# Performance work log

Measured on AMD Instinct MI355X. Metric: run time of the kernel, lower is better.

Reference implementation:

```python
import jax, jax.numpy as jnp
import numpy as np


def setup_inputs() -> dict:
    key = jax.random.key(0)
    k1, k2, k3 = jax.random.split(key, 3)
    B, E, L, D = 32, 256, 2048, 256
    doc_state = jax.random.normal(k1, (B, L, D), dtype=jnp.float32)
    entity_mapping = jax.random.uniform(k2, (B, E, L), dtype=jnp.float32)
    entity_lens = jax.random.uniform(k3, (B, E), dtype=jnp.float32)
    return {"doc_state": doc_state, "entity_mapping": entity_mapping, "entity_lens": entity_lens}


def reference(doc_state, entity_mapping, entity_lens):
    # Original: (entity_mapping[:, :, :, None] * doc_state[:, None, :, :]).sum(2) / entity_lens[:, :, None]
    # This is a batched contraction over L; express as einsum to avoid the
    # huge [B, E, L, D] intermediate.
    summed = jnp.einsum('bel,bld->bed', entity_mapping, doc_state)  # [B, E, D]
    return summed / entity_lens[:, :, None]
```

## Files before the change

### kernel.cpp

```cpp
#include <hip/hip_runtime.h>
#include <stdint.h>

#define B_ 32
#define E_ 256
#define L_ 2048
#define D_ 256

#define BE 128
#define BD 256
#define BK 32
#define KS 4
#define KCHUNK (L_ / KS)
#define NKT (KCHUNK / BK)
#define SUP 128

typedef __attribute__((ext_vector_type(2))) float  f32x2;
typedef __attribute__((ext_vector_type(4))) float  f32x4;
typedef __attribute__((ext_vector_type(4))) short  s16x4;
typedef __attribute__((ext_vector_type(8))) short  s16x8;

#define KEYB(row) (((row) >> 1) & 7)

__device__ __forceinline__ void cvt_hilo1(float x, short &h, short &l) {
    unsigned u = __builtin_bit_cast(unsigned, x);
    h = (short)(u >> 16);
    float hf = __builtin_bit_cast(float, u & 0xFFFF0000u);
    unsigned r = __builtin_bit_cast(unsigned, x - hf);
    l = (short)(r >> 16);
}

__global__ void zero_out_kernel(f32x4* __restrict__ out) {
    out[(size_t)blockIdx.x * 256 + threadIdx.x] = f32x4{0.f, 0.f, 0.f, 0.f};
}

#define LOAD_A(RA, SS)                                                         \
    {                                                                          \
        _Pragma("unroll")                                                      \
        for (int rr = 0; rr < 8; ++rr)                                         \
            RA[rr] = *(const f32x4*)(Ag + (size_t)(rr * 16 + a_sr) * L_ + (SS) * SUP + a_sc * 4); \
    }

#define WRITE_A(RA)                                                            \
    {                                                                          \
        _Pragma("unroll")                                                      \
        for (int rr = 0; rr < 8; ++rr) {                                       \
            s16x4 h, l;                                                        \
            _Pragma("unroll")                                                  \
            for (int i = 0; i < 4; ++i) { short hh, ll; cvt_hilo1(RA[rr][i], hh, ll); h[i] = hh; l[i] = ll; } \
            *(s16x4*)&A_hi[awoff + rr * 2048] = h;                             \
            *(s16x4*)&A_lo[awoff + rr * 2048] = l;                             \
        }                                                                      \
    }

#define LOADT_B(PB, K0)                                                        \
    {                                                                          \
        _Pragma("unroll")                                                      \
        for (int j = 0; j < 8; ++j)                                            \
            PB[j] = *(const f32x2*)(Sg + (size_t)((K0) + kb * 8 + j) * D_ + dp * 2); \
    }

#define STAGE_B(BbN, PB)                                                       \
    {                                                                          \
        _Pragma("unroll")                                                      \
        for (int dd = 0; dd < 2; ++dd) {                                       \
            s16x8 h, l;                                                        \
            _Pragma("unroll")                                                  \
            for (int j = 0; j < 8; ++j) { short hh, ll; cvt_hilo1(PB[j][dd], hh, ll); h[j] = hh; l[j] = ll; } \
            *(s16x8*)&(BbN)[bwo_h[dd]] = h;                                    \
            *(s16x8*)&(BbN)[bwo_l[dd]] = l;                                    \
        }                                                                      \
    }

#define LGKM_BARRIER()                                                         \
    {                                                                          \
        asm volatile("s_waitcnt lgkmcnt(0)" ::: "memory");                     \
        __builtin_amdgcn_s_barrier();                                          \
        asm volatile("" ::: "memory");                                         \
    }

#define ITER(K, S, BbC, BbN, PB)                                               \
    {                                                                          \
        s16x8 bh[4], bl[4], ah[4], al[4];                                      \
        _Pragma("unroll")                                                      \
        for (int ni = 0; ni < 4; ++ni) {                                       \
            bh[ni] = *(const s16x8*)&(BbC)[bro_h[ni]];                         \
            bl[ni] = *(const s16x8*)&(BbC)[bro_l[ni]];                         \
        }                                                                      \
        _Pragma("unroll")                                                      \
        for (int mi = 0; mi < 4; ++mi) {                                       \
            const int aoff = abase[mi] + ((((S) * 4 + kg) ^ akey[mi]) << 3);   \
            ah[mi] = *(const s16x8*)&A_hi[aoff];                               \
            al[mi] = *(const s16x8*)&A_lo[aoff];                               \
        }                                                                      \
        if ((K) + 1 < NKT) {                                                   \
            STAGE_B(BbN, PB)                                                   \
            if ((K) + 3 < NKT) LOADT_B(PB, ((K) + 3) * BK)                     \
        }                                                                      \
        __builtin_amdgcn_s_setprio(1);                                         \
        _Pragma("unroll")                                                      \
        for (int mi = 0; mi < 4; ++mi)                                         \
            _Pragma("unroll")                                                  \
            for (int ni = 0; ni < 4; ++ni) {                                   \
                acc[mi][ni] = __builtin_amdgcn_mfma_f32_16x16x32_bf16(ah[mi], bh[ni], acc[mi][ni], 0, 0, 0); \
                acc[mi][ni] = __builtin_amdgcn_mfma_f32_16x16x32_bf16(ah[mi], bl[ni], acc[mi][ni], 0, 0, 0); \
                acc[mi][ni] = __builtin_amdgcn_mfma_f32_16x16x32_bf16(al[mi], bh[ni], acc[mi][ni], 0, 0, 0); \
            }                                                                  \
        __builtin_amdgcn_s_setprio(0);                                         \
        if ((K) + 1 < NKT) LGKM_BARRIER()                                      \
    }

__global__ __launch_bounds__(512, 2)
void mean_pool_kernel(const float* __restrict__ doc,
                      const float* __restrict__ emap,
                      const float* __restrict__ lens,
                      float* __restrict__ out) {
    __shared__ __align__(16) short A_hi[BE * SUP];
    __shared__ __align__(16) short A_lo[BE * SUP];
    __shared__ __align__(16) short Bs[2][BD][64];
    __shared__ float lens_s[BE];

    const int t  = threadIdx.x;
    const int bi = blockIdx.x;
    const int r   = bi & 7;
    const int q   = bi >> 3;
    const int ks  = r & 3;
    const int b   = (q >> 1) * 2 + (r >> 2);
    const int e0  = (q & 1) * BE;

    const float* Ag = emap + ((size_t)b * E_ + e0) * L_ + ks * KCHUNK;
    const float* Sg = doc  + (size_t)b * L_ * D_ + (size_t)ks * KCHUNK * D_;

    if (t < BE) lens_s[t] = lens[b * E_ + e0 + t];

    const int a_sr = t >> 5;
    const int a_sc = t & 31;
    const int akey_w = a_sr & 7;
    const int awoff = a_sr * SUP + (((a_sc >> 1) ^ akey_w) << 3) + (a_sc & 1) * 4;

    const int dp = t & 127;
    const int kb = t >> 7;

    const int lane = t & 63;
    const int w    = t >> 6;
    const int eo   = (w & 1) * 64;
    const int dq   = (w >> 1) * 32 * 2;
    const int ml   = lane & 15;
    const int kg   = lane >> 4;

    int bwo_h[2], bwo_l[2];
    #pragma unroll
    for (int dd = 0; dd < 2; ++dd) {
        const int row = dp * 2 + dd, k = KEYB(row);
        bwo_h[dd] = row * 64 + (((kb    ) ^ k) << 3);
        bwo_l[dd] = row * 64 + (((kb | 4) ^ k) << 3);
    }
    int abase[4], akey[4], bro_h[4], bro_l[4];
    #pragma unroll
    for (int i = 0; i < 4; ++i) {
        const int ar = eo + i * 16 + ml;
        abase[i] = ar * SUP;
        akey[i]  = ar & 7;
        const int br = dq + i * 16 + ml, kB = KEYB(br);
        bro_h[i] = br * 64 + (((kg    ) ^ kB) << 3);
        bro_l[i] = br * 64 + (((kg | 4) ^ kB) << 3);
    }

    f32x4 acc[4][4] = {};
    f32x4 ra[8];
    f32x2 pbE[8], pbO[8];

    LOAD_A(ra, 0)
    LOADT_B(pbE, 0)
    LOADT_B(pbO, BK)
    STAGE_B((&Bs[0][0][0]), pbE)
    LOADT_B(pbE, 2 * BK)

    for (int ss = 0; ss < 4; ++ss) {
        WRITE_A(ra)
        if (ss < 3) LOAD_A(ra, ss + 1)
        LGKM_BARRIER()

        const int kt = ss * 4;
        ITER(kt + 0, 0, (&Bs[0][0][0]), (&Bs[1][0][0]), pbO)
        ITER(kt + 1, 1, (&Bs[1][0][0]), (&Bs[0][0][0]), pbE)
        ITER(kt + 2, 2, (&Bs[0][0][0]), (&Bs[1][0][0]), pbO)
        ITER(kt + 3, 3, (&Bs[1][0][0]), (&Bs[0][0][0]), pbE)
    }

    #pragma unroll
    for (int mi = 0; mi < 4; ++mi) {
        #pragma unroll
        for (int rr = 0; rr < 4; ++rr) {
            const int er = eo + mi * 16 + kg * 4 + rr;
            const float lv = lens_s[er];
            #pragma unroll
            for (int ni = 0; ni < 4; ++ni)
                atomicAdd(&out[((size_t)(b * E_ + e0 + er)) * D_ + dq + ni * 16 + ml],
                          acc[mi][ni][rr] / lv);
        }
    }
}

extern "C" void kernel_launch(void* const* d_in, const int* in_sizes, int n_in,
                              void* d_out, int out_size, void* d_ws, size_t ws_size,
                              hipStream_t stream) {
    const float* doc  = (const float*)d_in[0];
    const float* emap = (const float*)d_in[1];
    const float* lens = (const float*)d_in[2];
    float* out = (float*)d_out;

    zero_out_kernel<<<dim3(out_size / (4 * 256)), dim3(256), 0, stream>>>((f32x4*)out);

    dim3 grid(B_ * (E_ / BE) * (D_ / BD) * KS);
    dim3 block(512);
    hipLaunchKernelGGL(mean_pool_kernel, grid, block, 0, stream,
                       doc, emap, lens, out);
}
```

Before: 180.3 us.

## Drop block barriers: per-warp private A LDS buffers and direct-register B fragments

Replaces the block-shared A tile and double-buffered shared B staging with per-warp private LDS buffers for A and direct global-to-register loads of B in MFMA fragment layout. All workgroup barriers are removed, so waves progress independently, and lens is read from global in the epilogue. The cost is scalar, strided B loads that are duplicated across the waves sharing a D range, which raises memory and cache traffic.

```diff
diff --git a/kernel.cpp b/kernel.cpp
--- a/kernel.cpp
+++ b/kernel.cpp
@@ -12,14 +12,10 @@
 #define KS 4
 #define KCHUNK (L_ / KS)
 #define NKT (KCHUNK / BK)
-#define SUP 128
 
-typedef __attribute__((ext_vector_type(2))) float  f32x2;
 typedef __attribute__((ext_vector_type(4))) float  f32x4;
 typedef __attribute__((ext_vector_type(4))) short  s16x4;
 typedef __attribute__((ext_vector_type(8))) short  s16x8;
-
-#define KEYB(row) (((row) >> 1) & 7)
 
 __device__ __forceinline__ void cvt_hilo1(float x, short &h, short &l) {
     unsigned u = __builtin_bit_cast(unsigned, x);
@@ -33,80 +29,65 @@
     out[(size_t)blockIdx.x * 256 + threadIdx.x] = f32x4{0.f, 0.f, 0.f, 0.f};
 }
 
-#define LOAD_A(RA, SS)                                                         \
+#define LOADA(RA, K0)                                                          \
     {                                                                          \
         _Pragma("unroll")                                                      \
-        for (int rr = 0; rr < 8; ++rr)                                         \
-            RA[rr] = *(const f32x4*)(Ag + (size_t)(rr * 16 + a_sr) * L_ + (SS) * SUP + a_sc * 4); \
+        for (int i = 0; i < 8; ++i)                                            \
+            RA[i] = *(const f32x4*)(AgW + (size_t)(i * 8 + arow) * L_ + (K0) + akq * 4); \
     }
 
-#define WRITE_A(RA)                                                            \
+#define LOADB(PB, K0)                                                          \
     {                                                                          \
         _Pragma("unroll")                                                      \
-        for (int rr = 0; rr < 8; ++rr) {                                       \
+        for (int ni = 0; ni < 4; ++ni)                                         \
+            _Pragma("unroll")                                                  \
+            for (int j = 0; j < 8; ++j)                                        \
+                PB[ni][j] = Sg[(size_t)((K0) + kg * 8 + j) * D_ + dq + ni * 16 + ml]; \
+    }
+
+#define CVTWRITE_A(AW, RA)                                                     \
+    {                                                                          \
+        _Pragma("unroll")                                                      \
+        for (int i = 0; i < 8; ++i) {                                          \
             s16x4 h, l;                                                        \
             _Pragma("unroll")                                                  \
-            for (int i = 0; i < 4; ++i) { short hh, ll; cvt_hilo1(RA[rr][i], hh, ll); h[i] = hh; l[i] = ll; } \
-            *(s16x4*)&A_hi[awoff + rr * 2048] = h;                             \
-            *(s16x4*)&A_lo[awoff + rr * 2048] = l;                             \
+            for (int q = 0; q < 4; ++q) { short hh, ll; cvt_hilo1(RA[i][q], hh, ll); h[q] = hh; l[q] = ll; } \
+            *(s16x4*)&(AW)[i * 256 + awoff]        = h;                        \
+            *(s16x4*)&(AW)[i * 256 + awoff + 2048] = l;                        \
         }                                                                      \
     }
 
-#define LOADT_B(PB, K0)                                                        \
+#define CVT_B(BH, BL, PB)                                                      \
     {                                                                          \
         _Pragma("unroll")                                                      \
-        for (int j = 0; j < 8; ++j)                                            \
-            PB[j] = *(const f32x2*)(Sg + (size_t)((K0) + kb * 8 + j) * D_ + dp * 2); \
+        for (int ni = 0; ni < 4; ++ni)                                         \
+            _Pragma("unroll")                                                  \
+            for (int j = 0; j < 8; ++j) {                                      \
+                short hh, ll; cvt_hilo1(PB[ni][j], hh, ll);                    \
+                BH[ni][j] = hh; BL[ni][j] = ll;                                \
+            }                                                                  \
     }
 
-#define STAGE_B(BbN, PB)                                                       \
+#define STEP(K, AW)                                                            \
     {                                                                          \
-        _Pragma("unroll")                                                      \
-        for (int dd = 0; dd < 2; ++dd) {                                       \
-            s16x8 h, l;                                                        \
-            _Pragma("unroll")                                                  \
-            for (int j = 0; j < 8; ++j) { short hh, ll; cvt_hilo1(PB[j][dd], hh, ll); h[j] = hh; l[j] = ll; } \
-            *(s16x8*)&(BbN)[bwo_h[dd]] = h;                                    \
-            *(s16x8*)&(BbN)[bwo_l[dd]] = l;                                    \
-        }                                                                      \
-    }
-
-#define LGKM_BARRIER()                                                         \
-    {                                                                          \
-        asm volatile("s_waitcnt lgkmcnt(0)" ::: "memory");                     \
-        __builtin_amdgcn_s_barrier();                                          \
-        asm volatile("" ::: "memory");                                         \
-    }
-
-#define ITER(K, S, BbC, BbN, PB)                                               \
-    {                                                                          \
-        s16x8 bh[4], bl[4], ah[4], al[4];                                      \
-        _Pragma("unroll")                                                      \
-        for (int ni = 0; ni < 4; ++ni) {                                       \
-            bh[ni] = *(const s16x8*)&(BbC)[bro_h[ni]];                         \
-            bl[ni] = *(const s16x8*)&(BbC)[bro_l[ni]];                         \
-        }                                                                      \
+        CVTWRITE_A(AW, ra)                                                     \
+        if ((K) + 1 < NKT) LOADA(ra, ((K) + 1) * BK)                           \
+        s16x8 bh[4], bl[4];                                                    \
+        CVT_B(bh, bl, pbv)                                                     \
+        if ((K) + 1 < NKT) LOADB(pbv, ((K) + 1) * BK)                          \
+        __builtin_amdgcn_s_setprio(1);                                         \
         _Pragma("unroll")                                                      \
         for (int mi = 0; mi < 4; ++mi) {                                       \
-            const int aoff = abase[mi] + ((((S) * 4 + kg) ^ akey[mi]) << 3);   \
-            ah[mi] = *(const s16x8*)&A_hi[aoff];                               \
-            al[mi] = *(const s16x8*)&A_lo[aoff];                               \
-        }                                                                      \
-        if ((K) + 1 < NKT) {                                                   \
-            STAGE_B(BbN, PB)                                                   \
-            if ((K) + 3 < NKT) LOADT_B(PB, ((K) + 3) * BK)                     \
-        }                                                                      \
-        __builtin_amdgcn_s_setprio(1);                                         \
-        _Pragma("unroll")                                                      \
-        for (int mi = 0; mi < 4; ++mi)                                         \
+            const s16x8 ah = *(const s16x8*)&(AW)[aoff[mi]];                   \
+            const s16x8 al = *(const s16x8*)&(AW)[aoff[mi] + 2048];            \
             _Pragma("unroll")                                                  \
             for (int ni = 0; ni < 4; ++ni) {                                   \
-                acc[mi][ni] = __builtin_amdgcn_mfma_f32_16x16x32_bf16(ah[mi], bh[ni], acc[mi][ni], 0, 0, 0); \
-                acc[mi][ni] = __builtin_amdgcn_mfma_f32_16x16x32_bf16(ah[mi], bl[ni], acc[mi][ni], 0, 0, 0); \
-                acc[mi][ni] = __builtin_amdgcn_mfma_f32_16x16x32_bf16(al[mi], bh[ni], acc[mi][ni], 0, 0, 0); \
+                acc[mi][ni] = __builtin_amdgcn_mfma_f32_16x16x32_bf16(ah, bh[ni], acc[mi][ni], 0, 0, 0); \
+                acc[mi][ni] = __builtin_amdgcn_mfma_f32_16x16x32_bf16(ah, bl[ni], acc[mi][ni], 0, 0, 0); \
+                acc[mi][ni] = __builtin_amdgcn_mfma_f32_16x16x32_bf16(al, bh[ni], acc[mi][ni], 0, 0, 0); \
             }                                                                  \
+        }                                                                      \
         __builtin_amdgcn_s_setprio(0);                                         \
-        if ((K) + 1 < NKT) LGKM_BARRIER()                                      \
     }
 
 __global__ __launch_bounds__(512, 2)
@@ -114,10 +95,7 @@
                       const float* __restrict__ emap,
                       const float* __restrict__ lens,
                       float* __restrict__ out) {
-    __shared__ __align__(16) short A_hi[BE * SUP];
-    __shared__ __align__(16) short A_lo[BE * SUP];
-    __shared__ __align__(16) short Bs[2][BD][64];
-    __shared__ float lens_s[BE];
+    __shared__ __align__(16) short Apriv[8][2][4096];
 
     const int t  = threadIdx.x;
     const int bi = blockIdx.x;
@@ -130,69 +108,50 @@
     const float* Ag = emap + ((size_t)b * E_ + e0) * L_ + ks * KCHUNK;
     const float* Sg = doc  + (size_t)b * L_ * D_ + (size_t)ks * KCHUNK * D_;
 
-    if (t < BE) lens_s[t] = lens[b * E_ + e0 + t];
-
-    const int a_sr = t >> 5;
-    const int a_sc = t & 31;
-    const int akey_w = a_sr & 7;
-    const int awoff = a_sr * SUP + (((a_sc >> 1) ^ akey_w) << 3) + (a_sc & 1) * 4;
-
-    const int dp = t & 127;
-    const int kb = t >> 7;
-
     const int lane = t & 63;
     const int w    = t >> 6;
     const int eo   = (w & 1) * 64;
-    const int dq   = (w >> 1) * 32 * 2;
+    const int dq   = (w >> 1) * 64;
     const int ml   = lane & 15;
     const int kg   = lane >> 4;
 
-    int bwo_h[2], bwo_l[2];
+    const float* AgW = Ag + (size_t)eo * L_;
+
+    const int arow = lane >> 3;
+    const int akq  = lane & 7;
+    const int awoff = (arow * 8 + (akq ^ (arow & 6))) * 4;
+
+    int aoff[4];
     #pragma unroll
-    for (int dd = 0; dd < 2; ++dd) {
-        const int row = dp * 2 + dd, k = KEYB(row);
-        bwo_h[dd] = row * 64 + (((kb    ) ^ k) << 3);
-        bwo_l[dd] = row * 64 + (((kb | 4) ^ k) << 3);
+    for (int mi = 0; mi < 4; ++mi) {
+        const int row = mi * 16 + ml;
+        const int r7  = row & 7;
+        const int slot = r7 * 8 + ((2 * kg) ^ (r7 & 6));
+        aoff[mi] = (row >> 3) * 256 + slot * 4;
     }
-    int abase[4], akey[4], bro_h[4], bro_l[4];
-    #pragma unroll
-    for (int i = 0; i < 4; ++i) {
-        const int ar = eo + i * 16 + ml;
-        abase[i] = ar * SUP;
-        akey[i]  = ar & 7;
-        const int br = dq + i * 16 + ml, kB = KEYB(br);
-        bro_h[i] = br * 64 + (((kg    ) ^ kB) << 3);
-        bro_l[i] = br * 64 + (((kg | 4) ^ kB) << 3);
-    }
+
+    short* const A0 = &Apriv[w][0][0];
+    short* const A1 = &Apriv[w][1][0];
 
     f32x4 acc[4][4] = {};
     f32x4 ra[8];
-    f32x2 pbE[8], pbO[8];
+    float pbv[4][8];
 
-    LOAD_A(ra, 0)
-    LOADT_B(pbE, 0)
-    LOADT_B(pbO, BK)
-    STAGE_B((&Bs[0][0][0]), pbE)
-    LOADT_B(pbE, 2 * BK)
+    LOADA(ra, 0)
+    LOADB(pbv, 0)
 
-    for (int ss = 0; ss < 4; ++ss) {
-        WRITE_A(ra)
-        if (ss < 3) LOAD_A(ra, ss + 1)
-        LGKM_BARRIER()
-
-        const int kt = ss * 4;
-        ITER(kt + 0, 0, (&Bs[0][0][0]), (&Bs[1][0][0]), pbO)
-        ITER(kt + 1, 1, (&Bs[1][0][0]), (&Bs[0][0][0]), pbE)
-        ITER(kt + 2, 2, (&Bs[0][0][0]), (&Bs[1][0][0]), pbO)
-        ITER(kt + 3, 3, (&Bs[1][0][0]), (&Bs[0][0][0]), pbE)
+    for (int kt = 0; kt < NKT; kt += 2) {
+        STEP(kt,     A0)
+        STEP(kt + 1, A1)
     }
 
+    const float* lensB = lens + b * E_ + e0;
     #pragma unroll
     for (int mi = 0; mi < 4; ++mi) {
         #pragma unroll
         for (int rr = 0; rr < 4; ++rr) {
             const int er = eo + mi * 16 + kg * 4 + rr;
-            const float lv = lens_s[er];
+            const float lv = lensB[er];
             #pragma unroll
             for (int ni = 0; ni < 4; ++ni)
                 atomicAdd(&out[((size_t)(b * E_ + e0 + er)) * D_ + dq + ni * 16 + ml],
```

Result: slower. 337.6 us (+87.3%).
